# Kernel optimization log

Hardware: AMD Instinct MI355X
Metric: run time of the kernel (lower is better)

## Reference

```python
import jax, jax.numpy as jnp
import numpy as np

RATE_CHOICE = np.array([32, 64, 96, 128, 160, 192, 224, 256], dtype=np.int32)
B, C, S = 8, 256, 2048
RATE_NUM = len(RATE_CHOICE)
MAX_R = int(RATE_CHOICE.max())  # == C, required by residual add


def setup_inputs() -> dict:
    key = jax.random.key(0)
    k1, k2, k3, k4 = jax.random.split(key, 4)
    x = jax.random.normal(k1, (B, C, S), dtype=jnp.float32)
    indexes = jax.random.randint(k2, (B * S,), 0, RATE_NUM, dtype=jnp.int64)
    # kaiming-normal-ish weight, uniform bias as in the torch init
    weight = jax.random.normal(k3, (RATE_NUM, C, MAX_R), dtype=jnp.float32) * (1.0 / np.sqrt(C))
    bound = 1.0 / np.sqrt(C)
    bias = jax.random.uniform(k4, (RATE_NUM, MAX_R), dtype=jnp.float32, minval=-bound, maxval=bound)
    rate_choice = jnp.asarray(RATE_CHOICE)
    return {"x": x, "indexes": indexes, "weight": weight, "bias": bias, "rate_choice": rate_choice}


def reference(x, indexes, weight, bias, rate_choice):
    b_, c_, s_ = x.shape
    max_r = weight.shape[-1]
    x_blc = jnp.transpose(x, (0, 2, 1))              # (B, S, C)
    idx = indexes.reshape(b_, s_).astype(jnp.int32)  # (B, S)
    # Dense per-expert GEMM then select expert per token (same math as
    # index_select(weight, indexes) followed by per-token matmul, but avoids
    # materializing the (B,S,C,maxR) gathered weight tensor).
    all_proj = jnp.einsum('bsc,rcm->bsrm', x_blc, weight)        # (B, S, R, maxR)
    proj = jnp.take_along_axis(all_proj, idx[:, :, None, None], axis=2)[:, :, 0, :]  # (B, S, maxR)
    btok = bias[idx]                                             # (B, S, maxR)
    rc = rate_choice[idx]                                        # (B, S)
    mask = (jnp.arange(max_r)[None, None, :] < rc[:, :, None]).astype(x.dtype)  # (B, S, maxR)
    y = (x_blc + proj + btok) * mask                             # (B, S, maxR); maxR == C
    x_masked = jnp.transpose(y, (0, 2, 1))       # (B, maxR, S)
    mask_bchw = jnp.transpose(mask, (0, 2, 1))   # (B, maxR, S)
    return x_masked, mask_bchw, indexes
```

## Files before the change

kernel.cpp:

```cpp
#include <hip/hip_runtime.h>

#define B_ 8
#define C_ 256
#define S_ 2048
#define T_ (B_*S_)

typedef short s8v __attribute__((ext_vector_type(8)));
typedef short s4v __attribute__((ext_vector_type(4)));
typedef float f4v __attribute__((ext_vector_type(4)));

__device__ inline short f2b(float f){
  unsigned u = __builtin_bit_cast(unsigned, f);
  unsigned r = (u + 0x7FFFu + ((u >> 16) & 1u)) >> 16;
  return (short)r;
}
__device__ inline float b2f(short s){
  unsigned u = ((unsigned)(unsigned short)s) << 16;
  return __builtin_bit_cast(float, u);
}

__global__ __launch_bounds__(256) void k_pre(const float* __restrict__ x, short* __restrict__ xT,
                                             const float* __restrict__ wgt, short* __restrict__ wT2,
                                             const int* __restrict__ idx, int* __restrict__ counts,
                                             int* __restrict__ bucket, float* __restrict__ idx_out){
  __shared__ float tile[64][65];
  __shared__ int lcount[8];
  __shared__ int lbase[8];
  int tid = threadIdx.x;
  int bid = blockIdx.x;

  if (bid < 1024){
    int b  = bid >> 7;
    int ct = (bid >> 5) & 3;
    int st = bid & 31;
    const float* xb = x + b*(C_*S_);
    #pragma unroll
    for (int it = 0; it < 4; ++it){
      int row = it*16 + (tid >> 4);
      int s4  = tid & 15;
      float4 v = *(const float4*)(xb + (ct*64 + row)*S_ + st*64 + s4*4);
      tile[row][s4*4+0] = v.x; tile[row][s4*4+1] = v.y;
      tile[row][s4*4+2] = v.z; tile[row][s4*4+3] = v.w;
    }
    __syncthreads();
    #pragma unroll
    for (int it = 0; it < 4; ++it){
      int srow = it*16 + (tid >> 4);
      int c4   = tid & 15;
      s4v o;
      o[0] = f2b(tile[c4*4+0][srow]); o[1] = f2b(tile[c4*4+1][srow]);
      o[2] = f2b(tile[c4*4+2][srow]); o[3] = f2b(tile[c4*4+3][srow]);
      *(s4v*)(xT + (b*S_ + st*64 + srow)*C_ + ct*64 + c4*4) = o;
    }
  } else if (bid < 1152){
    int wb_ = bid - 1024;
    int r  = wb_ >> 4;
    int ct = (wb_ >> 2) & 3;
    int mt = wb_ & 3;
    const float* wsrc = wgt + r*(C_*256);
    #pragma unroll
    for (int it = 0; it < 4; ++it){
      int row = it*16 + (tid >> 4);
      int m4  = tid & 15;
      float4 v = *(const float4*)(wsrc + (ct*64 + row)*256 + mt*64 + m4*4);
      tile[row][m4*4+0] = v.x; tile[row][m4*4+1] = v.y;
      tile[row][m4*4+2] = v.z; tile[row][m4*4+3] = v.w;
    }
    __syncthreads();
    char* wdst = (char*)wT2 + r*131072;
    #pragma unroll
    for (int it = 0; it < 2; ++it){
      int q  = it*256 + tid;
      int ml = q >> 3;
      int ck = q & 7;
      int mg = mt*64 + ml;
      int cg = ct*64 + ck*8;
      int kcb = cg >> 5, klocal = cg & 31;
      s8v o;
      #pragma unroll
      for (int j = 0; j < 8; ++j) o[j] = f2b(tile[ck*8 + j][ml]);
      *(s8v*)(wdst + kcb*16384 + mg*64 + klocal*2) = o;
    }
  } else {
    int t = (bid - 1152)*256 + tid;
    if (tid < 8) lcount[tid] = 0;
    __syncthreads();
    int ei = idx[t];
    int e  = ei & 7;
    int lp = atomicAdd(&lcount[e], 1);
    __syncthreads();
    if (tid < 8){
      int c = lcount[tid];
      lbase[tid] = c ? atomicAdd(counts + tid, c) : 0;
    }
    __syncthreads();
    bucket[e*T_ + lbase[e] + lp] = t;
    idx_out[t] = (float)ei;
  }
}

__global__ __launch_bounds__(256,2) void k_gemm(const short* __restrict__ xT, const short* __restrict__ wT2,
                                                const float* __restrict__ bias, const int* __restrict__ counts,
                                                const int* __restrict__ bucket, const int* __restrict__ rate,
                                                short* __restrict__ yT){
  int e    = blockIdx.x >> 6;
  int slot = blockIdx.x & 63;
  int cnt  = counts[e];

  __shared__ short A [32*256];
  __shared__ short OS[32*256];
  __shared__ float biasS[256];
  __shared__ int   toks[32];

  int tid  = threadIdx.x;
  int lane = tid & 63, wv = tid >> 6;
  int l15  = lane & 15, lq = lane >> 4;

  biasS[tid] = bias[e*256 + tid];
  int rate_e = rate[e];
  const char* wTe = (const char*)wT2 + e*131072;
  char* AB  = (char*)A;
  char* OSB = (char*)OS;

  for (int tile = slot; tile*32 < cnt; tile += 64){
    int rowsV = cnt - tile*32; if (rowsV > 32) rowsV = 32;
    __syncthreads();
    if (tid < 32)
      toks[tid] = bucket[e*T_ + tile*32 + (tid < rowsV ? tid : rowsV - 1)];
    __syncthreads();

    {
      int row = tid >> 3, ck = tid & 7;
      const char* src = (const char*)xT + toks[row]*512 + ck*64;
      s8v v0 = *(const s8v*)(src);
      s8v v1 = *(const s8v*)(src + 16);
      s8v v2 = *(const s8v*)(src + 32);
      s8v v3 = *(const s8v*)(src + 48);
      int base = row*512, swz = (row & 7) << 4;
      *(s8v*)(AB + base + ((ck*64 +  0) ^ swz)) = v0;
      *(s8v*)(AB + base + ((ck*64 + 16) ^ swz)) = v1;
      *(s8v*)(AB + base + ((ck*64 + 32) ^ swz)) = v2;
      *(s8v*)(AB + base + ((ck*64 + 48) ^ swz)) = v3;
    }
    __syncthreads();

    f4v acc[2][4];
    #pragma unroll
    for (int mi = 0; mi < 2; ++mi)
      #pragma unroll
      for (int ni = 0; ni < 4; ++ni) acc[mi][ni] = (f4v){0.f,0.f,0.f,0.f};

    int aswz = (l15 & 7) << 4;
    #pragma unroll
    for (int kc = 0; kc < 8; ++kc){
      s8v a0 = *(const s8v*)(AB + l15*512        + ((kc*64 + lq*16) ^ aswz));
      s8v a1 = *(const s8v*)(AB + (16 + l15)*512 + ((kc*64 + lq*16) ^ aswz));
      #pragma unroll
      for (int ni = 0; ni < 4; ++ni){
        int n = wv*64 + ni*16 + l15;
        s8v bv = *(const s8v*)(wTe + kc*16384 + n*64 + lq*16);
        acc[0][ni] = __builtin_amdgcn_mfma_f32_16x16x32_bf16(a0, bv, acc[0][ni], 0, 0, 0);
        acc[1][ni] = __builtin_amdgcn_mfma_f32_16x16x32_bf16(a1, bv, acc[1][ni], 0, 0, 0);
      }
    }

    #pragma unroll
    for (int mi = 0; mi < 2; ++mi){
      #pragma unroll
      for (int ni = 0; ni < 4; ++ni){
        int col = wv*64 + ni*16 + l15;
        float bs = biasS[col];
        bool keep = col < rate_e;
        #pragma unroll
        for (int r = 0; r < 4; ++r){
          int row = mi*16 + lq*4 + r;
          float xres = b2f(*(const short*)(AB + row*512 + ((col*2) ^ ((row & 7) << 4))));
          float val  = keep ? (acc[mi][ni][r] + xres + bs) : 0.0f;
          *(short*)(OSB + row*512 + ((col*2) ^ ((row & 3) << 5))) = f2b(val);
        }
      }
    }
    __syncthreads();
    #pragma unroll
    for (int r2 = 0; r2 < 4; ++r2){
      int q = r2*4096 + tid*16;
      int row = q >> 9, off = q & 511;
      if (row < rowsV)
        *(s8v*)((char*)yT + toks[row]*512 + (off ^ ((row & 3) << 5))) = *(const s8v*)(OSB + q);
    }
  }
}

__global__ __launch_bounds__(256) void k_final(const short* __restrict__ yT, const int* __restrict__ idx,
                                               const int* __restrict__ rate_choice,
                                               float* __restrict__ outx, float* __restrict__ outm){
  int bid = blockIdx.x;
  int b  = bid >> 7;
  int ct = (bid >> 5) & 3;
  int st = bid & 31;
  __shared__ float tile[64][65];
  __shared__ int rateS[64];
  int tid = threadIdx.x;
  if (tid < 64) rateS[tid] = rate_choice[idx[b*S_ + st*64 + tid] & 7] >> 5;
  #pragma unroll
  for (int it = 0; it < 4; ++it){
    int srow = it*16 + (tid >> 4);
    int c4   = tid & 15;
    s4v v = *(const s4v*)(yT + (b*S_ + st*64 + srow)*C_ + ct*64 + c4*4);
    tile[c4*4+0][srow] = b2f(v[0]); tile[c4*4+1][srow] = b2f(v[1]);
    tile[c4*4+2][srow] = b2f(v[2]); tile[c4*4+3][srow] = b2f(v[3]);
  }
  __syncthreads();
  #pragma unroll
  for (int it = 0; it < 16; ++it){
    int cl = it*4 + (tid >> 6);
    int sl = tid & 63;
    int cg = ct*64 + cl;
    float v = tile[cl][sl];
    bool keep = (cg >> 5) < rateS[sl];
    int off = b*(C_*S_) + cg*S_ + st*64 + sl;
    outx[off] = v;
    outm[off] = keep ? 1.0f : 0.0f;
  }
}

extern "C" void kernel_launch(void* const* d_in, const int* in_sizes, int n_in,
                              void* d_out, int out_size, void* d_ws, size_t ws_size,
                              hipStream_t stream){
  const float* x    = (const float*)d_in[0];
  const int*   idx  = (const int*)d_in[1];
  const float* wgt  = (const float*)d_in[2];
  const float* bias = (const float*)d_in[3];
  const int*   rate = (const int*)d_in[4];

  char* ws = (char*)d_ws;
  short* xT     = (short*)ws;
  short* wT2    = (short*)(ws + 8388608);
  int*   bucket = (int*)  (ws + 9437184);
  int*   counts = (int*)  (ws + 9961472);
  short* yT     = (short*)(ws + 10485760);

  float* outx    = (float*)d_out;
  float* outm    = outx + (B_*C_*S_);
  float* idx_out = outx + 2*(B_*C_*S_);

  hipMemsetAsync(counts, 0, 32, stream);
  k_pre  <<<1216, 256, 0, stream>>>(x, xT, wgt, wT2, idx, counts, bucket, idx_out);
  k_gemm <<<512,  256, 0, stream>>>(xT, wT2, bias, counts, bucket, rate, yT);
  k_final<<<1024, 256, 0, stream>>>(yT, idx, rate, outx, outm);
}
```

Measured before the change: 40.15 us.

## Replace global expert buckets with per-segment local buckets to drop memset and atomics

Token routing now writes a per-256-token segment bucket sorted by expert with local counts, instead of global atomics into per-expert buckets. The GEMM kernel assigns one block per (segment, expert) pair and reads that segment's sublist, which removes the memset launch and global atomics. In exchange, tiles are smaller and partly empty, since each (segment, expert) holds about 32 tokens and rarely fills a 32-row tile exactly. The MFMA tiles therefore carry more padding waste, and the load balance across blocks changes.

```diff
diff --git a/kernel.cpp b/kernel.cpp
--- a/kernel.cpp
+++ b/kernel.cpp
@@ -21,11 +21,9 @@
 
 __global__ __launch_bounds__(256) void k_pre(const float* __restrict__ x, short* __restrict__ xT,
                                              const float* __restrict__ wgt, short* __restrict__ wT2,
-                                             const int* __restrict__ idx, int* __restrict__ counts,
-                                             int* __restrict__ bucket, float* __restrict__ idx_out){
+                                             const int* __restrict__ idx, int* __restrict__ segCnt,
+                                             int* __restrict__ segBucket, float* __restrict__ idx_out){
   __shared__ float tile[64][65];
-  __shared__ int lcount[8];
-  __shared__ int lbase[8];
   int tid = threadIdx.x;
   int bid = blockIdx.x;
 
@@ -82,30 +80,35 @@
       *(s8v*)(wdst + kcb*16384 + mg*64 + klocal*2) = o;
     }
   } else {
-    int t = (bid - 1152)*256 + tid;
+    int seg = bid - 1152;
+    __shared__ int lcount[8];
+    __shared__ int lbase[8];
+    int t = seg*256 + tid;
     if (tid < 8) lcount[tid] = 0;
     __syncthreads();
     int ei = idx[t];
     int e  = ei & 7;
     int lp = atomicAdd(&lcount[e], 1);
     __syncthreads();
-    if (tid < 8){
-      int c = lcount[tid];
-      lbase[tid] = c ? atomicAdd(counts + tid, c) : 0;
-    }
-    __syncthreads();
-    bucket[e*T_ + lbase[e] + lp] = t;
+    if (tid == 0){
+      int a0 = 0;
+      #pragma unroll
+      for (int e2 = 0; e2 < 8; ++e2){ lbase[e2] = a0; a0 += lcount[e2]; }
+    }
+    __syncthreads();
+    if (tid < 8) segCnt[seg*8 + tid] = lcount[tid];
+    segBucket[seg*256 + lbase[e] + lp] = t;
     idx_out[t] = (float)ei;
   }
 }
 
 __global__ __launch_bounds__(256,2) void k_gemm(const short* __restrict__ xT, const short* __restrict__ wT2,
-                                                const float* __restrict__ bias, const int* __restrict__ counts,
-                                                const int* __restrict__ bucket, const int* __restrict__ rate,
+                                                const float* __restrict__ bias, const int* __restrict__ segCnt,
+                                                const int* __restrict__ segBucket, const int* __restrict__ rate,
                                                 short* __restrict__ yT){
-  int e    = blockIdx.x >> 6;
-  int slot = blockIdx.x & 63;
-  int cnt  = counts[e];
+  int bid = blockIdx.x;
+  int e   = bid & 7;
+  int seg = bid >> 3;
 
   __shared__ short A [32*256];
   __shared__ short OS[32*256];
@@ -118,15 +121,25 @@
 
   biasS[tid] = bias[e*256 + tid];
   int rate_e = rate[e];
+
+  int off = 0, cnt = 0;
+  #pragma unroll
+  for (int j = 0; j < 8; ++j){
+    int c = segCnt[seg*8 + j];
+    if (j < e) off += c;
+    if (j == e) cnt = c;
+  }
+  const int* list = segBucket + seg*256 + off;
+
   const char* wTe = (const char*)wT2 + e*131072;
   char* AB  = (char*)A;
   char* OSB = (char*)OS;
 
-  for (int tile = slot; tile*32 < cnt; tile += 64){
-    int rowsV = cnt - tile*32; if (rowsV > 32) rowsV = 32;
+  for (int t0 = 0; t0 < cnt; t0 += 32){
+    int rowsV = cnt - t0; if (rowsV > 32) rowsV = 32;
     __syncthreads();
     if (tid < 32)
-      toks[tid] = bucket[e*T_ + tile*32 + (tid < rowsV ? tid : rowsV - 1)];
+      toks[tid] = list[t0 + (tid < rowsV ? tid : rowsV - 1)];
     __syncthreads();
 
     {
@@ -184,9 +197,9 @@
     #pragma unroll
     for (int r2 = 0; r2 < 4; ++r2){
       int q = r2*4096 + tid*16;
-      int row = q >> 9, off = q & 511;
+      int row = q >> 9, off2 = q & 511;
       if (row < rowsV)
-        *(s8v*)((char*)yT + toks[row]*512 + (off ^ ((row & 3) << 5))) = *(const s8v*)(OSB + q);
+        *(s8v*)((char*)yT + toks[row]*512 + (off2 ^ ((row & 3) << 5))) = *(const s8v*)(OSB + q);
     }
   }
 }
@@ -234,18 +247,17 @@
   const int*   rate = (const int*)d_in[4];
 
   char* ws = (char*)d_ws;
-  short* xT     = (short*)ws;
-  short* wT2    = (short*)(ws + 8388608);
-  int*   bucket = (int*)  (ws + 9437184);
-  int*   counts = (int*)  (ws + 9961472);
-  short* yT     = (short*)(ws + 10485760);
+  short* xT        = (short*)ws;
+  short* wT2       = (short*)(ws + 8388608);
+  int*   segBucket = (int*)  (ws + 9437184);
+  int*   segCnt    = (int*)  (ws + 9502720);
+  short* yT        = (short*)(ws + 10485760);
 
   float* outx    = (float*)d_out;
   float* outm    = outx + (B_*C_*S_);
   float* idx_out = outx + 2*(B_*C_*S_);
 
-  hipMemsetAsync(counts, 0, 32, stream);
-  k_pre  <<<1216, 256, 0, stream>>>(x, xT, wgt, wT2, idx, counts, bucket, idx_out);
-  k_gemm <<<512,  256, 0, stream>>>(xT, wT2, bias, counts, bucket, rate, yT);
+  k_pre  <<<1216, 256, 0, stream>>>(x, xT, wgt, wT2, idx, segCnt, segBucket, idx_out);
+  k_gemm <<<512,  256, 0, stream>>>(xT, wT2, bias, segCnt, segBucket, rate, yT);
   k_final<<<1024, 256, 0, stream>>>(yT, idx, rate, outx, outm);
 }
```

Result: faster. 35.29 us (median of 2 runs) (-12.1%).
